# Optimization experiments

Measured on AMD Instinct MI355X. Metric: run time of the kernel, lower is better.

## Reference

```python
import jax, jax.numpy as jnp
import numpy as np
from math import sqrt


def _init_linear(key, fan_in, fan_out, bias_fill=None):
    kw, kb = jax.random.split(key)
    s = 1.0 / np.sqrt(fan_in)
    W = jax.random.uniform(kw, (fan_in, fan_out), minval=-s, maxval=s, dtype=jnp.float32)
    if bias_fill is None:
        b = jax.random.uniform(kb, (fan_out,), minval=-s, maxval=s, dtype=jnp.float32)
    else:
        b = jnp.full((fan_out,), bias_fill, dtype=jnp.float32)
    return W, b


def setup_inputs() -> dict:
    key = jax.random.key(0)
    ks = jax.random.split(key, 16)
    N, P = 16, 4096
    C, H, W = 128, 28, 28
    G = 512  # global encoding dim
    inp = {}
    inp['points'] = jax.random.normal(ks[0], (N, P, 3), dtype=jnp.float32)
    inp['transform'] = 0.1 * jax.random.normal(ks[1], (N, P, 12), dtype=jnp.float32)
    inp['enc_filters'] = jax.random.normal(ks[2], (N, C, H, W), dtype=jnp.float32)
    inp['enc_glob'] = jax.random.normal(ks[3], (N, G), dtype=jnp.float32)
    # spat_mlp: 15 -> 128 -> 784 (one hidden layer)
    inp['sw1'], inp['sb1'] = _init_linear(ks[4], 3 + 12, 128)
    inp['sw2'], inp['sb2'] = _init_linear(ks[5], 128, H * W)
    # gate_mlp: 527 -> 128 -> 128, last bias init to 1
    inp['gw1'], inp['gb1'] = _init_linear(ks[6], G + 3 + 12, 128)
    inp['gw2'], inp['gb2'] = _init_linear(ks[7], 128, C, bias_fill=1.0)
    # fold mlp: 657 -> 128 -> 128 -> 3 (two hidden layers)
    D_in = C + G + 3 + 2 + 12
    inp['fw1'], inp['fb1'] = _init_linear(ks[8], D_in, 128)
    inp['fw2'], inp['fb2'] = _init_linear(ks[9], 128, 128)
    inp['fw3'], inp['fb3'] = _init_linear(ks[10], 128, 3)
    return inp


def _spatial_grid(k):
    # k x k grid in [-1, 1]^2, flattened to (k*k, 2)
    xs = jnp.linspace(-1.0, 1.0, k, dtype=jnp.float32)
    gx, gy = jnp.meshgrid(xs, xs, indexing='ij')
    return jnp.stack([gx.ravel(), gy.ravel()], axis=-1)


def _normalize_points(p):
    # center each cloud and scale to the unit sphere (max norm = 1)
    c = p - jnp.mean(p, axis=1, keepdims=True)
    scale = jnp.max(jnp.linalg.norm(c, axis=-1), axis=1, keepdims=True)  # (N,1)
    return c / (scale[..., None] + 1e-8)


def reference(points, transform, enc_filters, enc_glob,
              sw1, sb1, sw2, sb2, gw1, gb1, gw2, gb2,
              fw1, fb1, fw2, fb2, fw3, fb3):
    N, P, _ = points.shape
    _, C, H, W = enc_filters.shape
    G = enc_glob.shape[-1]
    factor = 1
    k = int(sqrt(P * factor))
    coords = jnp.broadcast_to(_spatial_grid(k)[None], (N, P * factor, 2))
    globs = jnp.broadcast_to(enc_glob[:, None, :], (N, P, G))
    code_vecs = jnp.concatenate([points, transform, globs], axis=-1)  # (N,P,527)
    # factor == 1 so repeat_interleave is identity
    fold_feats = jnp.concatenate([code_vecs, coords], axis=-1)  # (N,P,529)
    spat_in = fold_feats[:, :, : 3 + 12]
    gate_in = fold_feats[:, :, : 3 + 12 + G]
    # spatial attention over HW locations
    sh = jax.nn.relu(spat_in @ sw1 + sb1)
    sattn = jax.nn.softmax(sh @ sw2 + sb2, axis=-1)  # (N,P,HW)
    # channel gate
    gh = jax.nn.relu(gate_in @ gw1 + gb1)
    gattn = jax.nn.sigmoid(gh @ gw2 + gb2)  # (N,P,C)
    filters = enc_filters.reshape(N, C, H * W)
    spat_map = jnp.einsum('npq,ncq->npc', sattn, filters)  # fused weighted sum
    spat_feats = gattn * spat_map  # (N,P,C)
    inputs = jnp.concatenate([fold_feats, spat_feats], axis=-1)  # (N,P,657)
    h = jax.nn.relu(inputs @ fw1 + fb1)
    h = jax.nn.relu(h @ fw2 + fb2)
    deform = h @ fw3 + fb3  # (N,P,3)
    return _normalize_points(deform + inputs[:, :, :3])
```

## Files before the change

kernel.cpp:

```cpp
#include <hip/hip_runtime.h>
#include <hip/hip_bf16.h>

#define N_   16
#define P_   4096
#define C_   128
#define HW_  784
#define G_   512

typedef unsigned short u16;
typedef unsigned int   u32;
typedef __attribute__((ext_vector_type(8))) short bf16x8;
typedef __attribute__((ext_vector_type(4))) float f32x4;

union B8 { bf16x8 v; u32 w[4]; };

#define MFMA(a,b,c) __builtin_amdgcn_mfma_f32_16x16x32_bf16((a),(b),(c),0,0,0)

__device__ __forceinline__ u16 f2b(float f) {
    __hip_bfloat16 h = __float2bfloat16(f);
    return *reinterpret_cast<u16*>(&h);
}
__device__ __forceinline__ u32 pk(float lo, float hi) {
    return (u32)f2b(lo) | ((u32)f2b(hi) << 16);
}

#define OFF_SW2P    0
#define OFF_SW1P    204800
#define OFF_GW1P    212992
#define OFF_GW2P    221184
#define OFF_FW1BP   253952
#define OFF_FW2P    286720
#define OFF_SB2P    319488
#define OFF_GLOBGH  322688
#define OFF_GLOBF1  330880
#define OFF_FW1SP   339072
#define OFF_FW3P    347264
#define OFF_FILTP   349312

#define E0 102400
#define E1 110592
#define E2 118784
#define E3 135168
#define E4 151552
#define E5 167936
#define E6 168736
#define E7 185120
#define E8 189216
#define E9 189728
#define E10 1828128

__device__ __forceinline__ int perm_c(int row) {
    const int ct = row >> 4, r = row & 15;
    return 32 * (ct >> 1) + 8 * (r >> 2) + 4 * (ct & 1) + (r & 3);
}

__global__ __launch_bounds__(256) void k_prep(
    const float* __restrict__ sw1, const float* __restrict__ sw2,
    const float* __restrict__ sb2, const float* __restrict__ gw1,
    const float* __restrict__ gw2, const float* __restrict__ fw1,
    const float* __restrict__ fw2, const float* __restrict__ fw3,
    const float* __restrict__ filters, const float* __restrict__ enc_glob,
    u16* __restrict__ sw2p, u16* __restrict__ sw1p, u16* __restrict__ gw1p,
    u16* __restrict__ gw2p, u16* __restrict__ fw1bp, u16* __restrict__ fw2p,
    float* __restrict__ sb2p, u16* __restrict__ fw1sp, float* __restrict__ fw3p,
    u16* __restrict__ filtp,
    float* __restrict__ glob_gh, float* __restrict__ glob_f1)
{
    const int idx = blockIdx.x * 256 + threadIdx.x;
    if (idx < E0) {
        const int r_new = idx >> 7, c = idx & 127;
        const int kt = r_new >> 5, o = r_new & 31, h = (o >> 4) & 1, r = o & 15;
        const int q = kt * 32 + 8 * (r >> 2) + 4 * h + (r & 3);
        sw2p[idx] = (q < HW_) ? f2b(sw2[c * HW_ + q]) : (u16)0;
    } else if (idx < E1) {
        const int t = idx - E0;
        const int row = t >> 5, k = t & 31;
        const int c = perm_c(row);
        sw1p[t] = (k < 15) ? f2b(sw1[k * C_ + c]) : (u16)0;
    } else if (idx < E2) {
        const int t = idx - E1;
        const int row = t >> 5, k = t & 31;
        const int c = perm_c(row);
        gw1p[t] = (k < 15) ? f2b(gw1[k * C_ + c]) : (u16)0;
    } else if (idx < E3) {
        const int t = idx - E2;
        const int row = t >> 7, ci = t & 127;
        gw2p[t] = f2b(gw2[ci * C_ + perm_c(row)]);
    } else if (idx < E4) {
        const int t = idx - E3;
        const int row = t >> 7, ci = t & 127;
        fw1bp[t] = f2b(fw1[(529 + ci) * C_ + perm_c(row)]);
    } else if (idx < E5) {
        const int t = idx - E4;
        const int row = t >> 7, ci = t & 127;
        fw2p[t] = f2b(fw2[ci * C_ + perm_c(row)]);
    } else if (idx < E6) {
        const int q = idx - E5;
        sb2p[q] = (q < HW_) ? sb2[q] : -1e30f;
    } else if (idx < E7) {
        const int t = idx - E6;
        const int sub = t & 3, r = t >> 2;
        const int which = r >> 11, nn = (r >> 7) & 15, c = r & 127;
        const float* W = which ? fw1 : gw1;
        const float* gv = enc_glob + nn * G_ + sub * 128;
        const float* Wp = W + (15 + sub * 128) * C_ + c;
        float acc = 0.f;
        for (int k = 0; k < 128; ++k) acc += gv[k] * Wp[k * C_];
        acc += __shfl_xor(acc, 1);
        acc += __shfl_xor(acc, 2);
        if (sub == 0) (which ? glob_f1 : glob_gh)[nn * C_ + c] = acc;
    } else if (idx < E8) {
        const int t = idx - E7;
        const int row = t >> 5, k = t & 31;
        const int c = perm_c(row);
        float v = 0.f;
        if (k < 15)       v = fw1[k * C_ + c];
        else if (k == 15) v = fw1[527 * C_ + c];
        else if (k == 16) v = fw1[528 * C_ + c];
        fw1sp[t] = f2b(v);
    } else if (idx < E9) {
        const int t = idx - E8;
        const int row = t >> 2, j = t & 3;
        fw3p[t] = (j < 3) ? fw3[perm_c(row) * 3 + j] : 0.f;
    } else if (idx < E10) {
        const int t = idx - E9;
        const int nn = t / 102400;
        const int rr = t % 102400;
        const int row = rr / 800, q = rr % 800;
        const int c = perm_c(row);
        filtp[t] = (q < HW_) ? f2b(filters[((size_t)nn * C_ + c) * HW_ + q]) : (u16)0;
    }
}

__global__ __launch_bounds__(256, 2) void k_mfma(
    const float* __restrict__ points, const float* __restrict__ transform,
    const float* __restrict__ sb1, const float* __restrict__ gb1,
    const float* __restrict__ gb2, const float* __restrict__ fb1,
    const float* __restrict__ fb2, const float* __restrict__ fb3,
    const u16* __restrict__ sw1p, const u16* __restrict__ gw1p,
    const u16* __restrict__ sw2p, const float* __restrict__ sb2p,
    const u16* __restrict__ gw2p, const u16* __restrict__ fw1bp,
    const u16* __restrict__ fw2p, const u16* __restrict__ fw1sp,
    const float* __restrict__ fw3p, const u16* __restrict__ filtp,
    const float* __restrict__ glob_gh, const float* __restrict__ glob_f1,
    float* __restrict__ out)
{
    __shared__ __align__(16) float s_x[4][32][16];
    __shared__ __align__(16) u16 s_w[2][32][136];
    __shared__ __align__(16) u16 s_f[2][128][36];

    const int tid = threadIdx.x, wid = tid >> 6, lane = tid & 63;
    const int p = lane & 15, g = lane >> 4;
    const int bid = blockIdx.x;
    const int nb  = (bid & 7) * 64 + (bid >> 3);
    const int n   = nb >> 5;
    const int pw  = ((nb & 31) << 7) + (wid << 5);

    const u16* filtn = filtp + (size_t)n * 102400;
    const int swrow = tid >> 4, swc = tid & 15;
    const int frp   = tid >> 2, fc16 = tid & 3;

    for (int i = lane; i < 512; i += 64) {
        const int pt = i >> 4, k = i & 15;
        const int gp = n * P_ + pw + pt;
        float v = 0.f;
        if (k < 3)       v = points[gp * 3 + k];
        else if (k < 15) v = transform[gp * 12 + k - 3];
        s_x[wid][pt][k] = v;
    }

    {
        const bf16x8 w0 = *(const bf16x8*)(sw2p + (size_t)swrow * C_ + swc * 8);
        const bf16x8 w1 = *(const bf16x8*)(sw2p + (size_t)(16 + swrow) * C_ + swc * 8);
        const bf16x8 f0 = *(const bf16x8*)(filtn + (size_t)frp * 800 + fc16 * 8);
        const bf16x8 f1 = *(const bf16x8*)(filtn + (size_t)(64 + frp) * 800 + fc16 * 8);
        *(bf16x8*)&s_w[0][swrow][swc * 8]      = w0;
        *(bf16x8*)&s_w[0][16 + swrow][swc * 8] = w1;
        *(bf16x8*)&s_f[0][frp][fc16 * 8]       = f0;
        *(bf16x8*)&s_f[0][64 + frp][fc16 * 8]  = f1;
    }
    __syncthreads();

    B8 bxc[2];
    #pragma unroll
    for (int f = 0; f < 2; ++f) {
        bxc[f].w[0] = bxc[f].w[1] = bxc[f].w[2] = bxc[f].w[3] = 0u;
        const float* xs = &s_x[wid][p + 16 * f][0];
        const int pp = pw + p + 16 * f;
        const float cx = -1.f + 2.f * (float)(pp >> 6) / 63.f;
        const float cy = -1.f + 2.f * (float)(pp & 63) / 63.f;
        if (g == 0) {
            bxc[f].w[0] = pk(xs[0], xs[1]);  bxc[f].w[1] = pk(xs[2], xs[3]);
            bxc[f].w[2] = pk(xs[4], xs[5]);  bxc[f].w[3] = pk(xs[6], xs[7]);
        } else if (g == 1) {
            bxc[f].w[0] = pk(xs[8], xs[9]);  bxc[f].w[1] = pk(xs[10], xs[11]);
            bxc[f].w[2] = pk(xs[12], xs[13]); bxc[f].w[3] = pk(xs[14], cx);
        } else if (g == 2) {
            bxc[f].w[0] = pk(cy, 0.f);
        }
    }

    B8 bsh[4][2];
    #pragma unroll
    for (int ct = 0; ct < 8; ++ct) {
        const bf16x8 a_s = *(const bf16x8*)(sw1p + (16 * ct + p) * 32 + 8 * g);
        const int cb = 32 * (ct >> 1) + 8 * g + 4 * (ct & 1);
        const f32x4 b1 = *(const f32x4*)(sb1 + cb);
        const int m = ct >> 1, o = (ct & 1) * 2;
        #pragma unroll
        for (int f = 0; f < 2; ++f) {
            f32x4 cs = (f32x4){0.f, 0.f, 0.f, 0.f};
            cs = MFMA(a_s, bxc[f].v, cs);
            const float s0 = fmaxf(cs[0] + b1[0], 0.f), s1 = fmaxf(cs[1] + b1[1], 0.f);
            const float s2 = fmaxf(cs[2] + b1[2], 0.f), s3 = fmaxf(cs[3] + b1[3], 0.f);
            bsh[m][f].w[o] = pk(s0, s1); bsh[m][f].w[o + 1] = pk(s2, s3);
        }
    }

    f32x4 pv[8][2];
    #pragma unroll
    for (int ct = 0; ct < 8; ++ct)
        #pragma unroll
        for (int f = 0; f < 2; ++f) pv[ct][f] = (f32x4){0.f, 0.f, 0.f, 0.f};
    float psum0 = 0.f, psum1 = 0.f;

    for (int kt = 0; kt < 25; ++kt) {
        const int cur = kt & 1, nxt = cur ^ 1;
        bf16x8 stw0, stw1, stf0, stf1;
        if (kt < 24) {
            const int q0 = 32 * (kt + 1);
            stw0 = *(const bf16x8*)(sw2p + (size_t)(q0 + swrow) * C_ + swc * 8);
            stw1 = *(const bf16x8*)(sw2p + (size_t)(q0 + 16 + swrow) * C_ + swc * 8);
            stf0 = *(const bf16x8*)(filtn + (size_t)frp * 800 + q0 + fc16 * 8);
            stf1 = *(const bf16x8*)(filtn + (size_t)(64 + frp) * 800 + q0 + fc16 * 8);
        }

        B8 bq[2];
        #pragma unroll
        for (int h = 0; h < 2; ++h) {
            const u16* wr = &s_w[cur][16 * h + p][8 * g];
            const bf16x8 aw0 = *(const bf16x8*)(wr);
            const bf16x8 aw1 = *(const bf16x8*)(wr + 32);
            const bf16x8 aw2 = *(const bf16x8*)(wr + 64);
            const bf16x8 aw3 = *(const bf16x8*)(wr + 96);
            const f32x4 bi = *(const f32x4*)(sb2p + 32 * kt + 8 * g + 4 * h);
            #pragma unroll
            for (int f = 0; f < 2; ++f) {
                f32x4 c4 = (f32x4){0.f, 0.f, 0.f, 0.f};
                c4 = MFMA(aw0, bsh[0][f].v, c4);
                c4 = MFMA(aw1, bsh[1][f].v, c4);
                c4 = MFMA(aw2, bsh[2][f].v, c4);
                c4 = MFMA(aw3, bsh[3][f].v, c4);
                const float e0 = __expf(fminf(c4[0] + bi[0], 60.f));
                const float e1 = __expf(fminf(c4[1] + bi[1], 60.f));
                const float e2 = __expf(fminf(c4[2] + bi[2], 60.f));
                const float e3 = __expf(fminf(c4[3] + bi[3], 60.f));
                if (f == 0) psum0 += (e0 + e1) + (e2 + e3);
                else        psum1 += (e0 + e1) + (e2 + e3);
                bq[f].w[2 * h + 0] = pk(e0, e1);
                bq[f].w[2 * h + 1] = pk(e2, e3);
            }
        }
        #pragma unroll
        for (int ct = 0; ct < 8; ++ct) {
            const bf16x8 af = *(const bf16x8*)&s_f[cur][16 * ct + p][8 * g];
            pv[ct][0] = MFMA(af, bq[0].v, pv[ct][0]);
            pv[ct][1] = MFMA(af, bq[1].v, pv[ct][1]);
        }

        if (kt < 24) {
            *(bf16x8*)&s_w[nxt][swrow][swc * 8]      = stw0;
            *(bf16x8*)&s_w[nxt][16 + swrow][swc * 8] = stw1;
            *(bf16x8*)&s_f[nxt][frp][fc16 * 8]       = stf0;
            *(bf16x8*)&s_f[nxt][64 + frp][fc16 * 8]  = stf1;
        }
        __syncthreads();
    }
    psum0 += __shfl_xor(psum0, 16); psum0 += __shfl_xor(psum0, 32);
    psum1 += __shfl_xor(psum1, 16); psum1 += __shfl_xor(psum1, 32);
    const float inv0 = 1.f / psum0, inv1 = 1.f / psum1;

    B8 bgh[4][2];
    #pragma unroll
    for (int ct = 0; ct < 8; ++ct) {
        const bf16x8 a_g = *(const bf16x8*)(gw1p + (16 * ct + p) * 32 + 8 * g);
        const int cb = 32 * (ct >> 1) + 8 * g + 4 * (ct & 1);
        const f32x4 b2 = *(const f32x4*)(gb1 + cb);
        const f32x4 gg = *(const f32x4*)(glob_gh + n * C_ + cb);
        const int m = ct >> 1, o = (ct & 1) * 2;
        #pragma unroll
        for (int f = 0; f < 2; ++f) {
            f32x4 cg = (f32x4){0.f, 0.f, 0.f, 0.f};
            cg = MFMA(a_g, bxc[f].v, cg);
            const float g0 = fmaxf(cg[0] + b2[0] + gg[0], 0.f), g1 = fmaxf(cg[1] + b2[1] + gg[1], 0.f);
            const float g2 = fmaxf(cg[2] + b2[2] + gg[2], 0.f), g3 = fmaxf(cg[3] + b2[3] + gg[3], 0.f);
            bgh[m][f].w[o] = pk(g0, g1); bgh[m][f].w[o + 1] = pk(g2, g3);
        }
    }

    B8 bsf[4][2];
    #pragma unroll
    for (int ct = 0; ct < 8; ++ct) {
        const u16* ar = gw2p + (16 * ct + p) * C_ + 8 * g;
        const bf16x8 a0 = *(const bf16x8*)(ar),      a1 = *(const bf16x8*)(ar + 32);
        const bf16x8 a2 = *(const bf16x8*)(ar + 64), a3 = *(const bf16x8*)(ar + 96);
        const int cb = 32 * (ct >> 1) + 8 * g + 4 * (ct & 1);
        const f32x4 gb = *(const f32x4*)(gb2 + cb);
        const int m = ct >> 1, o = (ct & 1) * 2;
        #pragma unroll
        for (int f = 0; f < 2; ++f) {
            f32x4 acc = (f32x4){0.f, 0.f, 0.f, 0.f};
            acc = MFMA(a0, bgh[0][f].v, acc);
            acc = MFMA(a1, bgh[1][f].v, acc);
            acc = MFMA(a2, bgh[2][f].v, acc);
            acc = MFMA(a3, bgh[3][f].v, acc);
            const float iv = f ? inv1 : inv0;
            const float s0 = pv[ct][f][0] * iv / (1.f + __expf(-(acc[0] + gb[0])));
            const float s1 = pv[ct][f][1] * iv / (1.f + __expf(-(acc[1] + gb[1])));
            const float s2 = pv[ct][f][2] * iv / (1.f + __expf(-(acc[2] + gb[2])));
            const float s3 = pv[ct][f][3] * iv / (1.f + __expf(-(acc[3] + gb[3])));
            bsf[m][f].w[o] = pk(s0, s1); bsf[m][f].w[o + 1] = pk(s2, s3);
        }
    }

    B8 bh1[4][2];
    #pragma unroll
    for (int ct = 0; ct < 8; ++ct) {
        const u16* ar = fw1bp + (16 * ct + p) * C_ + 8 * g;
        const bf16x8 a0 = *(const bf16x8*)(ar),      a1 = *(const bf16x8*)(ar + 32);
        const bf16x8 a2 = *(const bf16x8*)(ar + 64), a3 = *(const bf16x8*)(ar + 96);
        const bf16x8 a_s = *(const bf16x8*)(fw1sp + (16 * ct + p) * 32 + 8 * g);
        const int cb = 32 * (ct >> 1) + 8 * g + 4 * (ct & 1);
        const f32x4 fbv = *(const f32x4*)(fb1 + cb);
        const f32x4 gf  = *(const f32x4*)(glob_f1 + n * C_ + cb);
        const int m = ct >> 1, o = (ct & 1) * 2;
        #pragma unroll
        for (int f = 0; f < 2; ++f) {
            f32x4 acc = (f32x4){0.f, 0.f, 0.f, 0.f};
            acc = MFMA(a0, bsf[0][f].v, acc);
            acc = MFMA(a1, bsf[1][f].v, acc);
            acc = MFMA(a2, bsf[2][f].v, acc);
            acc = MFMA(a3, bsf[3][f].v, acc);
            acc = MFMA(a_s, bxc[f].v, acc);
            const float h0 = fmaxf(acc[0] + fbv[0] + gf[0], 0.f);
            const float h1v = fmaxf(acc[1] + fbv[1] + gf[1], 0.f);
            const float h2 = fmaxf(acc[2] + fbv[2] + gf[2], 0.f);
            const float h3 = fmaxf(acc[3] + fbv[3] + gf[3], 0.f);
            bh1[m][f].w[o] = pk(h0, h1v); bh1[m][f].w[o + 1] = pk(h2, h3);
        }
    }

    float d0[2] = {0.f, 0.f}, d1[2] = {0.f, 0.f}, d2[2] = {0.f, 0.f};
    #pragma unroll
    for (int ct = 0; ct < 8; ++ct) {
        const u16* ar = fw2p + (16 * ct + p) * C_ + 8 * g;
        const bf16x8 a0 = *(const bf16x8*)(ar),      a1 = *(const bf16x8*)(ar + 32);
        const bf16x8 a2 = *(const bf16x8*)(ar + 64), a3 = *(const bf16x8*)(ar + 96);
        const int cb = 32 * (ct >> 1) + 8 * g + 4 * (ct & 1);
        const f32x4 o4 = *(const f32x4*)(fb2 + cb);
        f32x4 w3r[4];
        #pragma unroll
        for (int r = 0; r < 4; ++r)
            w3r[r] = *(const f32x4*)(fw3p + (16 * ct + 4 * g + r) * 4);
        #pragma unroll
        for (int f = 0; f < 2; ++f) {
            f32x4 acc = (f32x4){0.f, 0.f, 0.f, 0.f};
            acc = MFMA(a0, bh1[0][f].v, acc);
            acc = MFMA(a1, bh1[1][f].v, acc);
            acc = MFMA(a2, bh1[2][f].v, acc);
            acc = MFMA(a3, bh1[3][f].v, acc);
            #pragma unroll
            for (int r = 0; r < 4; ++r) {
                const float h = fmaxf(acc[r] + o4[r], 0.f);
                d0[f] += h * w3r[r][0];
                d1[f] += h * w3r[r][1];
                d2[f] += h * w3r[r][2];
            }
        }
    }
    #pragma unroll
    for (int f = 0; f < 2; ++f) {
        float a0 = d0[f], a1 = d1[f], a2 = d2[f];
        a0 += __shfl_xor(a0, 16); a0 += __shfl_xor(a0, 32);
        a1 += __shfl_xor(a1, 16); a1 += __shfl_xor(a1, 32);
        a2 += __shfl_xor(a2, 16); a2 += __shfl_xor(a2, 32);
        if (g == 0) {
            const int pt = p + 16 * f;
            const int gp = n * P_ + pw + pt;
            out[gp * 3 + 0] = a0 + fb3[0] + s_x[wid][pt][0];
            out[gp * 3 + 1] = a1 + fb3[1] + s_x[wid][pt][1];
            out[gp * 3 + 2] = a2 + fb3[2] + s_x[wid][pt][2];
        }
    }
}

__global__ __launch_bounds__(1024) void k_norm(float* __restrict__ out)
{
    __shared__ float red[48];
    __shared__ float red2[16];
    const int n = blockIdx.x, tid = threadIdx.x;
    float* pb = out + (size_t)n * P_ * 3;

    float sx = 0.f, sy = 0.f, sz = 0.f;
    for (int i = tid; i < P_; i += 1024) {
        sx += pb[i * 3 + 0]; sy += pb[i * 3 + 1]; sz += pb[i * 3 + 2];
    }
    #pragma unroll
    for (int m = 32; m >= 1; m >>= 1) {
        sx += __shfl_xor(sx, m); sy += __shfl_xor(sy, m); sz += __shfl_xor(sz, m);
    }
    const int wv = tid >> 6, ln = tid & 63;
    if (ln == 0) { red[wv * 3 + 0] = sx; red[wv * 3 + 1] = sy; red[wv * 3 + 2] = sz; }
    __syncthreads();
    float meanx = 0.f, meany = 0.f, meanz = 0.f;
    #pragma unroll
    for (int w = 0; w < 16; ++w) {
        meanx += red[w * 3 + 0]; meany += red[w * 3 + 1]; meanz += red[w * 3 + 2];
    }
    meanx /= (float)P_; meany /= (float)P_; meanz /= (float)P_;

    float mm = 0.f;
    for (int i = tid; i < P_; i += 1024) {
        const float dx = pb[i * 3 + 0] - meanx;
        const float dy = pb[i * 3 + 1] - meany;
        const float dz = pb[i * 3 + 2] - meanz;
        mm = fmaxf(mm, dx * dx + dy * dy + dz * dz);
    }
    #pragma unroll
    for (int m = 32; m >= 1; m >>= 1) mm = fmaxf(mm, __shfl_xor(mm, m));
    if (ln == 0) red2[wv] = mm;
    __syncthreads();
    mm = 0.f;
    #pragma unroll
    for (int w = 0; w < 16; ++w) mm = fmaxf(mm, red2[w]);
    const float scale = 1.f / (sqrtf(mm) + 1e-8f);

    for (int i = tid; i < P_; i += 1024) {
        pb[i * 3 + 0] = (pb[i * 3 + 0] - meanx) * scale;
        pb[i * 3 + 1] = (pb[i * 3 + 1] - meany) * scale;
        pb[i * 3 + 2] = (pb[i * 3 + 2] - meanz) * scale;
    }
}

extern "C" void kernel_launch(void* const* d_in, const int* in_sizes, int n_in,
                              void* d_out, int out_size, void* d_ws, size_t ws_size,
                              hipStream_t stream) {
    const float* points    = (const float*)d_in[0];
    const float* transform = (const float*)d_in[1];
    const float* filters   = (const float*)d_in[2];
    const float* enc_glob  = (const float*)d_in[3];
    const float* sw1 = (const float*)d_in[4];
    const float* sb1 = (const float*)d_in[5];
    const float* sw2 = (const float*)d_in[6];
    const float* sb2 = (const float*)d_in[7];
    const float* gw1 = (const float*)d_in[8];
    const float* gb1 = (const float*)d_in[9];
    const float* gw2 = (const float*)d_in[10];
    const float* gb2 = (const float*)d_in[11];
    const float* fw1 = (const float*)d_in[12];
    const float* fb1 = (const float*)d_in[13];
    const float* fw2 = (const float*)d_in[14];
    const float* fb2 = (const float*)d_in[15];
    const float* fw3 = (const float*)d_in[16];
    const float* fb3 = (const float*)d_in[17];

    char* ws = (char*)d_ws;
    u16*   sw2p    = (u16*)(ws + OFF_SW2P);
    u16*   sw1p    = (u16*)(ws + OFF_SW1P);
    u16*   gw1p    = (u16*)(ws + OFF_GW1P);
    u16*   gw2p    = (u16*)(ws + OFF_GW2P);
    u16*   fw1bp   = (u16*)(ws + OFF_FW1BP);
    u16*   fw2p    = (u16*)(ws + OFF_FW2P);
    float* sb2p    = (float*)(ws + OFF_SB2P);
    float* glob_gh = (float*)(ws + OFF_GLOBGH);
    float* glob_f1 = (float*)(ws + OFF_GLOBF1);
    u16*   fw1sp   = (u16*)(ws + OFF_FW1SP);
    float* fw3p    = (float*)(ws + OFF_FW3P);
    u16*   filtp   = (u16*)(ws + OFF_FILTP);
    float* out     = (float*)d_out;

    k_prep<<<(E10 + 255) / 256, 256, 0, stream>>>(
        sw1, sw2, sb2, gw1, gw2, fw1, fw2, fw3, filters, enc_glob,
        sw2p, sw1p, gw1p, gw2p, fw1bp, fw2p, sb2p, fw1sp, fw3p, filtp,
        glob_gh, glob_f1);
    k_mfma<<<N_ * (P_ / 128), 256, 0, stream>>>(
        points, transform, sb1, gb1, gb2, fb1, fb2, fb3,
        sw1p, gw1p, sw2p, sb2p, gw2p, fw1bp, fw2p, fw1sp, fw3p, filtp,
        glob_gh, glob_f1, out);
    k_norm<<<N_, 1024, 0, stream>>>(out);
}
```

Baseline: 171.3 us.

## Halve points per wave to cut registers and raise occupancy

Each wave now processes 16 points instead of 32, removing the second MFMA column per stage. This halves the accumulator and activation register arrays, and the launch bound is raised to 4 blocks per SM. The grid doubles to 1024 blocks. The trade-off is that every block now re-streams the sw2 and filter tiles through shared memory for half as many points, which doubles that global/LDS traffic and the per-point weight-load overhead.

```diff
diff --git a/kernel.cpp b/kernel.cpp
--- a/kernel.cpp
+++ b/kernel.cpp
@@ -132,7 +132,7 @@
     }
 }
 
-__global__ __launch_bounds__(256, 2) void k_mfma(
+__global__ __launch_bounds__(256, 4) void k_mfma(
     const float* __restrict__ points, const float* __restrict__ transform,
     const float* __restrict__ sb1, const float* __restrict__ gb1,
     const float* __restrict__ gb2, const float* __restrict__ fb1,
@@ -145,22 +145,22 @@
     const float* __restrict__ glob_gh, const float* __restrict__ glob_f1,
     float* __restrict__ out)
 {
-    __shared__ __align__(16) float s_x[4][32][16];
+    __shared__ __align__(16) float s_x[4][16][16];
     __shared__ __align__(16) u16 s_w[2][32][136];
     __shared__ __align__(16) u16 s_f[2][128][36];
 
     const int tid = threadIdx.x, wid = tid >> 6, lane = tid & 63;
     const int p = lane & 15, g = lane >> 4;
     const int bid = blockIdx.x;
-    const int nb  = (bid & 7) * 64 + (bid >> 3);
-    const int n   = nb >> 5;
-    const int pw  = ((nb & 31) << 7) + (wid << 5);
+    const int nb  = (bid & 7) * 128 + (bid >> 3);
+    const int n   = nb >> 6;
+    const int pw  = ((nb & 63) << 6) + (wid << 4);
 
     const u16* filtn = filtp + (size_t)n * 102400;
     const int swrow = tid >> 4, swc = tid & 15;
     const int frp   = tid >> 2, fc16 = tid & 3;
 
-    for (int i = lane; i < 512; i += 64) {
+    for (int i = lane; i < 256; i += 64) {
         const int pt = i >> 4, k = i & 15;
         const int gp = n * P_ + pw + pt;
         float v = 0.f;
@@ -181,48 +181,42 @@
     }
     __syncthreads();
 
-    B8 bxc[2];
-    #pragma unroll
-    for (int f = 0; f < 2; ++f) {
-        bxc[f].w[0] = bxc[f].w[1] = bxc[f].w[2] = bxc[f].w[3] = 0u;
-        const float* xs = &s_x[wid][p + 16 * f][0];
-        const int pp = pw + p + 16 * f;
+    B8 bxc;
+    bxc.w[0] = bxc.w[1] = bxc.w[2] = bxc.w[3] = 0u;
+    {
+        const float* xs = &s_x[wid][p][0];
+        const int pp = pw + p;
         const float cx = -1.f + 2.f * (float)(pp >> 6) / 63.f;
         const float cy = -1.f + 2.f * (float)(pp & 63) / 63.f;
         if (g == 0) {
-            bxc[f].w[0] = pk(xs[0], xs[1]);  bxc[f].w[1] = pk(xs[2], xs[3]);
-            bxc[f].w[2] = pk(xs[4], xs[5]);  bxc[f].w[3] = pk(xs[6], xs[7]);
+            bxc.w[0] = pk(xs[0], xs[1]);  bxc.w[1] = pk(xs[2], xs[3]);
+            bxc.w[2] = pk(xs[4], xs[5]);  bxc.w[3] = pk(xs[6], xs[7]);
         } else if (g == 1) {
-            bxc[f].w[0] = pk(xs[8], xs[9]);  bxc[f].w[1] = pk(xs[10], xs[11]);
-            bxc[f].w[2] = pk(xs[12], xs[13]); bxc[f].w[3] = pk(xs[14], cx);
+            bxc.w[0] = pk(xs[8], xs[9]);  bxc.w[1] = pk(xs[10], xs[11]);
+            bxc.w[2] = pk(xs[12], xs[13]); bxc.w[3] = pk(xs[14], cx);
         } else if (g == 2) {
-            bxc[f].w[0] = pk(cy, 0.f);
-        }
-    }
-
-    B8 bsh[4][2];
+            bxc.w[0] = pk(cy, 0.f);
+        }
+    }
+
+    B8 bsh[4];
     #pragma unroll
     for (int ct = 0; ct < 8; ++ct) {
         const bf16x8 a_s = *(const bf16x8*)(sw1p + (16 * ct + p) * 32 + 8 * g);
         const int cb = 32 * (ct >> 1) + 8 * g + 4 * (ct & 1);
         const f32x4 b1 = *(const f32x4*)(sb1 + cb);
         const int m = ct >> 1, o = (ct & 1) * 2;
-        #pragma unroll
-        for (int f = 0; f < 2; ++f) {
-            f32x4 cs = (f32x4){0.f, 0.f, 0.f, 0.f};
-            cs = MFMA(a_s, bxc[f].v, cs);
-            const float s0 = fmaxf(cs[0] + b1[0], 0.f), s1 = fmaxf(cs[1] + b1[1], 0.f);
-            const float s2 = fmaxf(cs[2] + b1[2], 0.f), s3 = fmaxf(cs[3] + b1[3], 0.f);
-            bsh[m][f].w[o] = pk(s0, s1); bsh[m][f].w[o + 1] = pk(s2, s3);
-        }
-    }
-
-    f32x4 pv[8][2];
-    #pragma unroll
-    for (int ct = 0; ct < 8; ++ct)
-        #pragma unroll
-        for (int f = 0; f < 2; ++f) pv[ct][f] = (f32x4){0.f, 0.f, 0.f, 0.f};
-    float psum0 = 0.f, psum1 = 0.f;
+        f32x4 cs = (f32x4){0.f, 0.f, 0.f, 0.f};
+        cs = MFMA(a_s, bxc.v, cs);
+        const float s0 = fmaxf(cs[0] + b1[0], 0.f), s1 = fmaxf(cs[1] + b1[1], 0.f);
+        const float s2 = fmaxf(cs[2] + b1[2], 0.f), s3 = fmaxf(cs[3] + b1[3], 0.f);
+        bsh[m].w[o] = pk(s0, s1); bsh[m].w[o + 1] = pk(s2, s3);
+    }
+
+    f32x4 pv[8];
+    #pragma unroll
+    for (int ct = 0; ct < 8; ++ct) pv[ct] = (f32x4){0.f, 0.f, 0.f, 0.f};
+    float psum = 0.f;
 
     for (int kt = 0; kt < 25; ++kt) {
         const int cur = kt & 1, nxt = cur ^ 1;
@@ -235,7 +229,7 @@
             stf1 = *(const bf16x8*)(filtn + (size_t)(64 + frp) * 800 + q0 + fc16 * 8);
         }
 
-        B8 bq[2];
+        B8 bq;
         #pragma unroll
         for (int h = 0; h < 2; ++h) {
             const u16* wr = &s_w[cur][16 * h + p][8 * g];
@@ -244,28 +238,23 @@
             const bf16x8 aw2 = *(const bf16x8*)(wr + 64);
             const bf16x8 aw3 = *(const bf16x8*)(wr + 96);
             const f32x4 bi = *(const f32x4*)(sb2p + 32 * kt + 8 * g + 4 * h);
-            #pragma unroll
-            for (int f = 0; f < 2; ++f) {
-                f32x4 c4 = (f32x4){0.f, 0.f, 0.f, 0.f};
-                c4 = MFMA(aw0, bsh[0][f].v, c4);
-                c4 = MFMA(aw1, bsh[1][f].v, c4);
-                c4 = MFMA(aw2, bsh[2][f].v, c4);
-                c4 = MFMA(aw3, bsh[3][f].v, c4);
-                const float e0 = __expf(fminf(c4[0] + bi[0], 60.f));
-                const float e1 = __expf(fminf(c4[1] + bi[1], 60.f));
-                const float e2 = __expf(fminf(c4[2] + bi[2], 60.f));
-                const float e3 = __expf(fminf(c4[3] + bi[3], 60.f));
-                if (f == 0) psum0 += (e0 + e1) + (e2 + e3);
-                else        psum1 += (e0 + e1) + (e2 + e3);
-                bq[f].w[2 * h + 0] = pk(e0, e1);
-                bq[f].w[2 * h + 1] = pk(e2, e3);
-            }
+            f32x4 c4 = (f32x4){0.f, 0.f, 0.f, 0.f};
+            c4 = MFMA(aw0, bsh[0].v, c4);
+            c4 = MFMA(aw1, bsh[1].v, c4);
+            c4 = MFMA(aw2, bsh[2].v, c4);
+            c4 = MFMA(aw3, bsh[3].v, c4);
+            const float e0 = __expf(fminf(c4[0] + bi[0], 60.f));
+            const float e1 = __expf(fminf(c4[1] + bi[1], 60.f));
+            const float e2 = __expf(fminf(c4[2] + bi[2], 60.f));
+            const float e3 = __expf(fminf(c4[3] + bi[3], 60.f));
+            psum += (e0 + e1) + (e2 + e3);
+            bq.w[2 * h + 0] = pk(e0, e1);
+            bq.w[2 * h + 1] = pk(e2, e3);
         }
         #pragma unroll
         for (int ct = 0; ct < 8; ++ct) {
             const bf16x8 af = *(const bf16x8*)&s_f[cur][16 * ct + p][8 * g];
-            pv[ct][0] = MFMA(af, bq[0].v, pv[ct][0]);
-            pv[ct][1] = MFMA(af, bq[1].v, pv[ct][1]);
+            pv[ct] = MFMA(af, bq.v, pv[ct]);
         }
 
         if (kt < 24) {
@@ -276,11 +265,11 @@
         }
         __syncthreads();
     }
-    psum0 += __shfl_xor(psum0, 16); psum0 += __shfl_xor(psum0, 32);
-    psum1 += __shfl_xor(psum1, 16); psum1 += __shfl_xor(psum1, 32);
-    const float inv0 = 1.f / psum0, inv1 = 1.f / psum1;
-
-    B8 bgh[4][2];
+    psum += __shfl_xor(psum, 16);
+    psum += __shfl_xor(psum, 32);
+    const float inv = 1.f / psum;
+
+    B8 bgh[4];
     #pragma unroll
     for (int ct = 0; ct < 8; ++ct) {
         const bf16x8 a_g = *(const bf16x8*)(gw1p + (16 * ct + p) * 32 + 8 * g);
@@ -288,109 +277,80 @@
         const f32x4 b2 = *(const f32x4*)(gb1 + cb);
         const f32x4 gg = *(const f32x4*)(glob_gh + n * C_ + cb);
         const int m = ct >> 1, o = (ct & 1) * 2;
-        #pragma unroll
-        for (int f = 0; f < 2; ++f) {
-            f32x4 cg = (f32x4){0.f, 0.f, 0.f, 0.f};
-            cg = MFMA(a_g, bxc[f].v, cg);
-            const float g0 = fmaxf(cg[0] + b2[0] + gg[0], 0.f), g1 = fmaxf(cg[1] + b2[1] + gg[1], 0.f);
-            const float g2 = fmaxf(cg[2] + b2[2] + gg[2], 0.f), g3 = fmaxf(cg[3] + b2[3] + gg[3], 0.f);
-            bgh[m][f].w[o] = pk(g0, g1); bgh[m][f].w[o + 1] = pk(g2, g3);
-        }
-    }
-
-    B8 bsf[4][2];
+        f32x4 cg = (f32x4){0.f, 0.f, 0.f, 0.f};
+        cg = MFMA(a_g, bxc.v, cg);
+        const float g0 = fmaxf(cg[0] + b2[0] + gg[0], 0.f), g1 = fmaxf(cg[1] + b2[1] + gg[1], 0.f);
+        const float g2 = fmaxf(cg[2] + b2[2] + gg[2], 0.f), g3 = fmaxf(cg[3] + b2[3] + gg[3], 0.f);
+        bgh[m].w[o] = pk(g0, g1); bgh[m].w[o + 1] = pk(g2, g3);
+    }
+
+    B8 bsf[4];
     #pragma unroll
     for (int ct = 0; ct < 8; ++ct) {
         const u16* ar = gw2p + (16 * ct + p) * C_ + 8 * g;
-        const bf16x8 a0 = *(const bf16x8*)(ar),      a1 = *(const bf16x8*)(ar + 32);
-        const bf16x8 a2 = *(const bf16x8*)(ar + 64), a3 = *(const bf16x8*)(ar + 96);
+        f32x4 acc = (f32x4){0.f, 0.f, 0.f, 0.f};
+        acc = MFMA(*(const bf16x8*)(ar),      bgh[0].v, acc);
+        acc = MFMA(*(const bf16x8*)(ar + 32), bgh[1].v, acc);
+        acc = MFMA(*(const bf16x8*)(ar + 64), bgh[2].v, acc);
+        acc = MFMA(*(const bf16x8*)(ar + 96), bgh[3].v, acc);
         const int cb = 32 * (ct >> 1) + 8 * g + 4 * (ct & 1);
         const f32x4 gb = *(const f32x4*)(gb2 + cb);
+        const float s0 = pv[ct][0] * inv / (1.f + __expf(-(acc[0] + gb[0])));
+        const float s1 = pv[ct][1] * inv / (1.f + __expf(-(acc[1] + gb[1])));
+        const float s2 = pv[ct][2] * inv / (1.f + __expf(-(acc[2] + gb[2])));
+        const float s3 = pv[ct][3] * inv / (1.f + __expf(-(acc[3] + gb[3])));
         const int m = ct >> 1, o = (ct & 1) * 2;
-        #pragma unroll
-        for (int f = 0; f < 2; ++f) {
-            f32x4 acc = (f32x4){0.f, 0.f, 0.f, 0.f};
-            acc = MFMA(a0, bgh[0][f].v, acc);
-            acc = MFMA(a1, bgh[1][f].v, acc);
-            acc = MFMA(a2, bgh[2][f].v, acc);
-            acc = MFMA(a3, bgh[3][f].v, acc);
-            const float iv = f ? inv1 : inv0;
-            const float s0 = pv[ct][f][0] * iv / (1.f + __expf(-(acc[0] + gb[0])));
-            const float s1 = pv[ct][f][1] * iv / (1.f + __expf(-(acc[1] + gb[1])));
-            const float s2 = pv[ct][f][2] * iv / (1.f + __expf(-(acc[2] + gb[2])));
-            const float s3 = pv[ct][f][3] * iv / (1.f + __expf(-(acc[3] + gb[3])));
-            bsf[m][f].w[o] = pk(s0, s1); bsf[m][f].w[o + 1] = pk(s2, s3);
-        }
-    }
-
-    B8 bh1[4][2];
+        bsf[m].w[o] = pk(s0, s1); bsf[m].w[o + 1] = pk(s2, s3);
+    }
+
+    B8 bh1[4];
     #pragma unroll
     for (int ct = 0; ct < 8; ++ct) {
         const u16* ar = fw1bp + (16 * ct + p) * C_ + 8 * g;
-        const bf16x8 a0 = *(const bf16x8*)(ar),      a1 = *(const bf16x8*)(ar + 32);
-        const bf16x8 a2 = *(const bf16x8*)(ar + 64), a3 = *(const bf16x8*)(ar + 96);
         const bf16x8 a_s = *(const bf16x8*)(fw1sp + (16 * ct + p) * 32 + 8 * g);
+        f32x4 acc = (f32x4){0.f, 0.f, 0.f, 0.f};
+        acc = MFMA(*(const bf16x8*)(ar),      bsf[0].v, acc);
+        acc = MFMA(*(const bf16x8*)(ar + 32), bsf[1].v, acc);
+        acc = MFMA(*(const bf16x8*)(ar + 64), bsf[2].v, acc);
+        acc = MFMA(*(const bf16x8*)(ar + 96), bsf[3].v, acc);
+        acc = MFMA(a_s, bxc.v, acc);
         const int cb = 32 * (ct >> 1) + 8 * g + 4 * (ct & 1);
         const f32x4 fbv = *(const f32x4*)(fb1 + cb);
         const f32x4 gf  = *(const f32x4*)(glob_f1 + n * C_ + cb);
+        const float h0 = fmaxf(acc[0] + fbv[0] + gf[0], 0.f);
+        const float h1v = fmaxf(acc[1] + fbv[1] + gf[1], 0.f);
+        const float h2 = fmaxf(acc[2] + fbv[2] + gf[2], 0.f);
+        const float h3 = fmaxf(acc[3] + fbv[3] + gf[3], 0.f);
         const int m = ct >> 1, o = (ct & 1) * 2;
-        #pragma unroll
-        for (int f = 0; f < 2; ++f) {
-            f32x4 acc = (f32x4){0.f, 0.f, 0.f, 0.f};
-            acc = MFMA(a0, bsf[0][f].v, acc);
-            acc = MFMA(a1, bsf[1][f].v, acc);
-            acc = MFMA(a2, bsf[2][f].v, acc);
-            acc = MFMA(a3, bsf[3][f].v, acc);
-            acc = MFMA(a_s, bxc[f].v, acc);
-            const float h0 = fmaxf(acc[0] + fbv[0] + gf[0], 0.f);
-            const float h1v = fmaxf(acc[1] + fbv[1] + gf[1], 0.f);
-            const float h2 = fmaxf(acc[2] + fbv[2] + gf[2], 0.f);
-            const float h3 = fmaxf(acc[3] + fbv[3] + gf[3], 0.f);
-            bh1[m][f].w[o] = pk(h0, h1v); bh1[m][f].w[o + 1] = pk(h2, h3);
-        }
-    }
-
-    float d0[2] = {0.f, 0.f}, d1[2] = {0.f, 0.f}, d2[2] = {0.f, 0.f};
+        bh1[m].w[o] = pk(h0, h1v); bh1[m].w[o + 1] = pk(h2, h3);
+    }
+
+    float d0 = 0.f, d1 = 0.f, d2 = 0.f;
     #pragma unroll
     for (int ct = 0; ct < 8; ++ct) {
         const u16* ar = fw2p + (16 * ct + p) * C_ + 8 * g;
-        const bf16x8 a0 = *(const bf16x8*)(ar),      a1 = *(const bf16x8*)(ar + 32);
-        const bf16x8 a2 = *(const bf16x8*)(ar + 64), a3 = *(const bf16x8*)(ar + 96);
+        f32x4 acc = (f32x4){0.f, 0.f, 0.f, 0.f};
+        acc = MFMA(*(const bf16x8*)(ar),      bh1[0].v, acc);
+        acc = MFMA(*(const bf16x8*)(ar + 32), bh1[1].v, acc);
+        acc = MFMA(*(const bf16x8*)(ar + 64), bh1[2].v, acc);
+        acc = MFMA(*(const bf16x8*)(ar + 96), bh1[3].v, acc);
         const int cb = 32 * (ct >> 1) + 8 * g + 4 * (ct & 1);
         const f32x4 o4 = *(const f32x4*)(fb2 + cb);
-        f32x4 w3r[4];
         #pragma unroll
-        for (int r = 0; r < 4; ++r)
-            w3r[r] = *(const f32x4*)(fw3p + (16 * ct + 4 * g + r) * 4);
-        #pragma unroll
-        for (int f = 0; f < 2; ++f) {
-            f32x4 acc = (f32x4){0.f, 0.f, 0.f, 0.f};
-            acc = MFMA(a0, bh1[0][f].v, acc);
-            acc = MFMA(a1, bh1[1][f].v, acc);
-            acc = MFMA(a2, bh1[2][f].v, acc);
-            acc = MFMA(a3, bh1[3][f].v, acc);
-            #pragma unroll
-            for (int r = 0; r < 4; ++r) {
-                const float h = fmaxf(acc[r] + o4[r], 0.f);
-                d0[f] += h * w3r[r][0];
-                d1[f] += h * w3r[r][1];
-                d2[f] += h * w3r[r][2];
-            }
-        }
-    }
-    #pragma unroll
-    for (int f = 0; f < 2; ++f) {
-        float a0 = d0[f], a1 = d1[f], a2 = d2[f];
-        a0 += __shfl_xor(a0, 16); a0 += __shfl_xor(a0, 32);
-        a1 += __shfl_xor(a1, 16); a1 += __shfl_xor(a1, 32);
-        a2 += __shfl_xor(a2, 16); a2 += __shfl_xor(a2, 32);
-        if (g == 0) {
-            const int pt = p + 16 * f;
-            const int gp = n * P_ + pw + pt;
-            out[gp * 3 + 0] = a0 + fb3[0] + s_x[wid][pt][0];
-            out[gp * 3 + 1] = a1 + fb3[1] + s_x[wid][pt][1];
-            out[gp * 3 + 2] = a2 + fb3[2] + s_x[wid][pt][2];
-        }
+        for (int r = 0; r < 4; ++r) {
+            const float h = fmaxf(acc[r] + o4[r], 0.f);
+            const f32x4 w3 = *(const f32x4*)(fw3p + (16 * ct + 4 * g + r) * 4);
+            d0 += h * w3[0]; d1 += h * w3[1]; d2 += h * w3[2];
+        }
+    }
+    d0 += __shfl_xor(d0, 16); d0 += __shfl_xor(d0, 32);
+    d1 += __shfl_xor(d1, 16); d1 += __shfl_xor(d1, 32);
+    d2 += __shfl_xor(d2, 16); d2 += __shfl_xor(d2, 32);
+    if (g == 0) {
+        const int gp = n * P_ + pw + p;
+        out[gp * 3 + 0] = d0 + fb3[0] + s_x[wid][p][0];
+        out[gp * 3 + 1] = d1 + fb3[1] + s_x[wid][p][1];
+        out[gp * 3 + 2] = d2 + fb3[2] + s_x[wid][p][2];
     }
 }
 
@@ -483,7 +443,7 @@
         sw1, sw2, sb2, gw1, gw2, fw1, fw2, fw3, filters, enc_glob,
         sw2p, sw1p, gw1p, gw2p, fw1bp, fw2p, sb2p, fw1sp, fw3p, filtp,
         glob_gh, glob_f1);
-    k_mfma<<<N_ * (P_ / 128), 256, 0, stream>>>(
+    k_mfma<<<N_ * (P_ / 64), 256, 0, stream>>>(
         points, transform, sb1, gb1, gb2, fb1, fb2, fb3,
         sw1p, gw1p, sw2p, sb2p, gw2p, fw1bp, fw2p, fw1sp, fw3p, filtp,
         glob_gh, glob_f1, out);
```

Result: slower. 203.3 us (+18.6%).
